# Kernel tuning notes

Measured on AMD Instinct MI355X. Metric: run time of the kernel, lower is better.

## Reference

```python
import jax, jax.numpy as jnp
import numpy as np
from math import factorial

LMAX = 2
M_TOT = (LMAX + 1) ** 2  # 9 real spherical-harmonic components
CUTOFF = 5.0
N_RBF = 20

# ---------- Clebsch-Gordan coefficients in the real-SH basis (static) ----------

def _cg(j1, m1, j2, m2, j3, m3):
    if m1 + m2 != m3 or not (abs(j1 - j2) <= j3 <= j1 + j2):
        return 0.0
    f = factorial
    pre = ((2 * j3 + 1) * f(j1 + j2 - j3) * f(j1 - j2 + j3) * f(-j1 + j2 + j3) / f(j1 + j2 + j3 + 1)) ** 0.5
    pre *= (f(j3 + m3) * f(j3 - m3) * f(j1 - m1) * f(j1 + m1) * f(j2 - m2) * f(j2 + m2)) ** 0.5
    s = 0.0
    for k in range(j1 + j2 + j3 + 1):
        den = [k, j1 + j2 - j3 - k, j1 - m1 - k, j2 + m2 - k, j3 - j2 + m1 + k, j3 - j1 - m2 + k]
        if min(den) < 0:
            continue
        t = 1.0
        for dd in den:
            t *= f(dd)
        s += (-1) ** k / t
    return pre * s

def _u_real(l):
    # complex -> real SH change of basis, rows: real m, cols: complex m (offset by l)
    U = np.zeros((2 * l + 1, 2 * l + 1), dtype=complex)
    U[l, l] = 1.0
    s2 = 1.0 / np.sqrt(2.0)
    for m in range(1, l + 1):
        U[l + m, l + m] = (-1) ** m * s2
        U[l + m, l - m] = s2
        U[l - m, l - m] = 1j * s2
        U[l - m, l + m] = -1j * (-1) ** m * s2
    return U

def _build_cg_real(lmax):
    n = (lmax + 1) ** 2
    cg = np.zeros((n, n, n))
    for l1 in range(lmax + 1):
        for l2 in range(lmax + 1):
            for l3 in range(lmax + 1):
                if not (abs(l1 - l2) <= l3 <= l1 + l2):
                    continue
                C = np.zeros((2 * l1 + 1, 2 * l2 + 1, 2 * l3 + 1), dtype=complex)
                for m1 in range(-l1, l1 + 1):
                    for m2 in range(-l2, l2 + 1):
                        m3 = m1 + m2
                        if abs(m3) <= l3:
                            C[m1 + l1, m2 + l2, m3 + l3] = _cg(l1, m1, l2, m2, l3, m3)
                Cr = np.einsum('ai,bj,ck,ijk->abc', _u_real(l1), _u_real(l2), _u_real(l3).conj(), C)
                # odd-parity (l1+l2+l3 odd) entries are purely imaginary -> Re() zeroes them
                cg[l1 * l1:(l1 + 1) ** 2, l2 * l2:(l2 + 1) ** 2, l3 * l3:(l3 + 1) ** 2] = Cr.real
    return cg

_CGD = _build_cg_real(LMAX)
_mask = np.abs(_CGD) > 1e-10
_i1, _i2, _io = np.nonzero(_mask)
IDX1, IDX2, IDXO = jnp.array(_i1), jnp.array(_i2), jnp.array(_io)
CG_VALS = jnp.array(_CGD[_mask].astype(np.float32))
_LS = np.concatenate([np.full(2 * l + 1, l) for l in range(LMAX + 1)])  # l of each flat (l,m) index
FILTER_IDX = jnp.array(_LS[_i2])  # radial filter channel = l of the spherical-harmonic input
LIDX = jnp.array(_LS)

# ---------- real spherical harmonics up to l=2 ----------

def rsh(d):  # d: [E,3] unit directions, output [E,9] ordered (l,m): (0,0),(1,-1..1),(2,-2..2)
    x, y, z = d[:, 0], d[:, 1], d[:, 2]
    c0 = 0.28209479177387814   # 0.5*sqrt(1/pi)
    c1 = 0.4886025119029199    # sqrt(3/(4*pi))
    c2 = 1.0925484305920792    # 0.5*sqrt(15/pi)
    c20 = 0.31539156525252005  # 0.25*sqrt(5/pi)
    c22 = 0.5462742152960396   # 0.25*sqrt(15/pi)
    return jnp.stack([
        jnp.full_like(x, c0),
        c1 * y, c1 * z, c1 * x,
        c2 * x * y, c2 * y * z, c20 * (3.0 * z * z - 1.0), c2 * x * z, c22 * (x * x - y * y),
    ], axis=-1)


def _forward(atomic_numbers, r_ij, idx_i, idx_j, emb, filt_w, filt_b,
             mix1_w, mix2_w, mix3_w, gate_w, gate_b):
    N = atomic_numbers.shape[0]
    F = emb.shape[-1]
    d = jnp.linalg.norm(r_ij, axis=1, keepdims=True)          # [E,1]
    dir_ij = r_ij / d
    Y = rsh(dir_ij)                                           # [E,9]
    offsets = jnp.linspace(0.0, CUTOFF, N_RBF)                # GaussianRBF
    coeff = -0.5 / (offsets[1] - offsets[0]) ** 2
    radial = jnp.exp(coeff * (d - offsets[None, 0:1] * 0 - offsets) ** 2)  # [E,n_rbf]
    cut = 0.5 * (jnp.cos(d * jnp.pi / CUTOFF) + 1.0) * (d < CUTOFF)        # CosineCutoff [E,1]
    x0 = emb[atomic_numbers]                                  # [N,F]
    x = jnp.concatenate([x0[:, None, :], jnp.zeros((N, M_TOT - 1, F), x0.dtype)], axis=1)  # scalar2rsh
    n_layers = filt_w.shape[0]
    for li in range(n_layers):
        # SO3Convolution: radial filter per output l, CG-coupled gather/scatter over edges
        W = (radial @ filt_w[li] + filt_b[li]).reshape(-1, LMAX + 1, F) * cut[:, :, None]  # [E,3,F]
        xj = x[idx_j]                                          # [E,9,F]
        v = xj[:, IDX1] * Y[:, IDX2, None] * CG_VALS[None, :, None] * W[:, FILTER_IDX]     # [E,P,F]
        v = jnp.zeros((v.shape[0], M_TOT, F), v.dtype).at[:, IDXO].add(v)                  # [E,9,F]
        dx = jax.ops.segment_sum(v, idx_i, num_segments=N)     # scatter to atoms [N,9,F]
        # mixing1 + SO3TensorProduct
        ddx = dx @ mix1_w[li]
        p = dx[:, IDX1] * ddx[:, IDX2] * CG_VALS[None, :, None]
        p = jnp.zeros((N, M_TOT, F), dx.dtype).at[:, IDXO].add(p)
        dx = dx + p
        # mixing2, parametric gated nonlinearity, mixing3
        dx = dx @ mix2_w[li]
        h = (dx[:, 0] @ gate_w[li] + gate_b[li]).reshape(N, LMAX + 1, F)
        dx = dx * jax.nn.sigmoid(h[:, LIDX])
        dx = dx @ mix3_w[li]
        x = x + dx
    return x  # multipole representation [N,9,F]; scalar rep is x[:,0]


def setup_inputs() -> dict:
    key = jax.random.key(0)
    ks = jax.random.split(key, 12)
    N, E, F, NR, L, MAXZ = 10000, 100000, 32, N_RBF, 2, 100
    atomic_numbers = jax.random.randint(ks[0], (N,), 0, MAXZ)
    r_ij = jax.random.normal(ks[1], (E, 3), dtype=jnp.float32)
    idx_i = jax.random.randint(ks[2], (E,), 0, N)
    idx_j = jax.random.randint(ks[3], (E,), 0, N)
    emb = jax.random.normal(ks[4], (MAXZ, F), dtype=jnp.float32)
    emb = emb.at[0].set(0.0)  # padding_idx=0
    filt_w = jax.random.normal(ks[5], (L, NR, (LMAX + 1) * F), dtype=jnp.float32) / np.sqrt(NR)
    filt_b = jnp.zeros((L, (LMAX + 1) * F), dtype=jnp.float32)
    mix1_w = jax.random.normal(ks[6], (L, F, F), dtype=jnp.float32) / np.sqrt(F)
    mix2_w = jax.random.normal(ks[7], (L, F, F), dtype=jnp.float32) / np.sqrt(F)
    mix3_w = jax.random.normal(ks[8], (L, F, F), dtype=jnp.float32) / np.sqrt(F)
    gate_w = jax.random.normal(ks[9], (L, F, (LMAX + 1) * F), dtype=jnp.float32) / np.sqrt(F)
    gate_b = jnp.zeros((L, (LMAX + 1) * F), dtype=jnp.float32)
    return {"atomic_numbers": atomic_numbers, "r_ij": r_ij, "idx_i": idx_i, "idx_j": idx_j,
            "emb": emb, "filt_w": filt_w, "filt_b": filt_b, "mix1_w": mix1_w,
            "mix2_w": mix2_w, "mix3_w": mix3_w, "gate_w": gate_w, "gate_b": gate_b}


def reference(atomic_numbers, r_ij, idx_i, idx_j, emb, filt_w, filt_b,
              mix1_w, mix2_w, mix3_w, gate_w, gate_b):
    return _forward(atomic_numbers, r_ij, idx_i, idx_j, emb, filt_w, filt_b,
                    mix1_w, mix2_w, mix3_w, gate_w, gate_b)
```

## Files before the change

### kernel.cpp

```cpp
#include <hip/hip_runtime.h>
#include <math.h>

#define F 32
#define NRBF 20
#define MAXNZ 192
#define MAXG 160
#define PI_F 3.14159265358979323846f

typedef float f4a __attribute__((ext_vector_type(4), aligned(4)));

constexpr double cfact(int n) { double r = 1.0; for (int i = 2; i <= n; i++) r *= (double)i; return r; }
constexpr double csqrt(double x) {
    if (x <= 0.0) return 0.0;
    double r = x < 1.0 ? 1.0 : x;
    for (int i = 0; i < 80; i++) r = 0.5 * (r + x / r);
    return r;
}
constexpr int cabs_i(int x) { return x < 0 ? -x : x; }

constexpr double cg_c(int j1, int m1, int j2, int m2, int j3, int m3) {
    if (m1 + m2 != m3) return 0.0;
    if (j3 < cabs_i(j1 - j2) || j3 > j1 + j2) return 0.0;
    double pre = csqrt((2.0 * j3 + 1) * cfact(j1 + j2 - j3) * cfact(j1 - j2 + j3) *
                       cfact(-j1 + j2 + j3) / cfact(j1 + j2 + j3 + 1));
    pre *= csqrt(cfact(j3 + m3) * cfact(j3 - m3) * cfact(j1 - m1) * cfact(j1 + m1) *
                 cfact(j2 - m2) * cfact(j2 + m2));
    double s = 0.0;
    for (int k = 0; k <= j1 + j2 + j3; k++) {
        int d0 = k, d1 = j1 + j2 - j3 - k, d2 = j1 - m1 - k, d3 = j2 + m2 - k;
        int d4 = j3 - j2 + m1 + k, d5 = j3 - j1 - m2 + k;
        if (d0 < 0 || d1 < 0 || d2 < 0 || d3 < 0 || d4 < 0 || d5 < 0) continue;
        double t = cfact(d0) * cfact(d1) * cfact(d2) * cfact(d3) * cfact(d4) * cfact(d5);
        s += ((k & 1) ? -1.0 : 1.0) / t;
    }
    return pre * s;
}

struct U5 { double re[5][5]; double im[5][5]; };
constexpr U5 u_real(int l) {
    U5 u{};
    u.re[l][l] = 1.0;
    double s2 = 1.0 / csqrt(2.0);
    for (int m = 1; m <= l; m++) {
        double sgn = (m & 1) ? -1.0 : 1.0;
        u.re[l + m][l + m] = sgn * s2;
        u.re[l + m][l - m] = s2;
        u.im[l - m][l - m] = s2;
        u.im[l - m][l + m] = -sgn * s2;
    }
    return u;
}

struct Dense { double c[9][9][9]; };
constexpr Dense build_dense() {
    Dense D{};
    for (int l1 = 0; l1 <= 2; l1++)
        for (int l2 = 0; l2 <= 2; l2++)
            for (int l3 = 0; l3 <= 2; l3++) {
                if (l3 < cabs_i(l1 - l2) || l3 > l1 + l2) continue;
                U5 U1 = u_real(l1), U2 = u_real(l2), U3 = u_real(l3);
                int n1 = 2 * l1 + 1, n2 = 2 * l2 + 1, n3 = 2 * l3 + 1;
                for (int i = 0; i < n1; i++)
                    for (int j = 0; j < n2; j++) {
                        int k = (i - l1) + (j - l2) + l3;
                        if (k < 0 || k >= n3) continue;
                        double C = cg_c(l1, i - l1, l2, j - l2, l3, k - l3);
                        if (C == 0.0) continue;
                        int as[2] = {i, n1 - 1 - i}, bs[2] = {j, n2 - 1 - j}, cs[2] = {k, n3 - 1 - k};
                        int na = (as[0] == as[1]) ? 1 : 2;
                        int nb = (bs[0] == bs[1]) ? 1 : 2;
                        int nc = (cs[0] == cs[1]) ? 1 : 2;
                        for (int ai = 0; ai < na; ai++)
                            for (int bi = 0; bi < nb; bi++)
                                for (int ci = 0; ci < nc; ci++) {
                                    int aa = as[ai], bb = bs[bi], cc = cs[ci];
                                    double xr = U1.re[aa][i], xi = U1.im[aa][i];
                                    double yr = U2.re[bb][j], yi = U2.im[bb][j];
                                    double tr = xr * yr - xi * yi;
                                    double ti = xr * yi + xi * yr;
                                    double zr = U3.re[cc][k], zi = -U3.im[cc][k];
                                    double add = (tr * zr - ti * zi) * C;
                                    if (add != 0.0)
                                        D.c[l1 * l1 + aa][l2 * l2 + bb][l3 * l3 + cc] += add;
                                }
                    }
            }
    return D;
}

struct CgG {
    int nnz, ng;
    int goff[10];
    int gb[MAXG];
    int aoff[MAXG + 1];
    int aidx[MAXNZ];
    float aval[MAXNZ];
};
constexpr CgG build_g() {
    CgG t{};
    Dense D = build_dense();
    int g = 0, c = 0;
    for (int o = 0; o < 9; o++) {
        t.goff[o] = g;
        for (int b = 0; b < 9; b++) {
            bool any = false;
            for (int a = 0; a < 9; a++) {
                double v = D.c[a][b][o];
                if (v > 1e-10 || v < -1e-10) {
                    if (!any) { t.gb[g] = b; t.aoff[g] = c; any = true; }
                    t.aidx[c] = a; t.aval[c] = (float)v; c++;
                }
            }
            if (any) g++;
        }
    }
    t.goff[9] = g; t.aoff[g] = c; t.ng = g; t.nnz = c;
    return t;
}
constexpr CgG CGG = build_g();
static_assert(CGG.nnz <= MAXNZ, "nnz overflow");
static_assert(CGG.ng <= MAXG, "group overflow");

struct CgF { int cnt; int b[16]; int o[16]; float v[16]; };
constexpr CgF build_f() {
    CgF t{};
    Dense D = build_dense();
    int c = 0;
    for (int o = 0; o < 9; o++)
        for (int b = 0; b < 9; b++) {
            double v = D.c[0][b][o];
            if (v > 1e-10 || v < -1e-10) { t.b[c] = b; t.o[c] = o; t.v[c] = (float)v; c++; }
        }
    t.cnt = c;
    return t;
}
constexpr CgF CGF = build_f();
static_assert(CGF.cnt <= 16, "first-layer table overflow");

__device__ inline float readlane_f(float v, int lane) {
    union { float f; int i; } u; u.f = v;
    int r = __builtin_amdgcn_readlane(u.i, lane);
    union { int i; float f; } w; w.i = r;
    return w.f;
}


__global__ void init_x_kernel(float* __restrict__ x, const int* __restrict__ Z,
                              const float* __restrict__ emb, int N) {
    int t = blockIdx.x * blockDim.x + threadIdx.x;
    if (t >= N * F) return;
    int n = t >> 5, f = t & 31;
    float* xp = x + (size_t)n * 288 + f * 9;
    xp[0] = emb[Z[n] * F + f];
    #pragma unroll
    for (int m = 1; m < 9; m++) xp[m] = 0.0f;
}

__global__ void hist_kernel(const int* __restrict__ idx_i, int* __restrict__ deg, int E) {
    int e = blockIdx.x * blockDim.x + threadIdx.x;
    if (e < E) atomicAdd(&deg[idx_i[e]], 1);
}

#define SCAN_T 1024
__global__ __launch_bounds__(SCAN_T) void scan_kernel(
    const int* __restrict__ deg, int* __restrict__ rowptr,
    int* __restrict__ cursor, int N) {
    __shared__ int part[SCAN_T];
    int t = threadIdx.x;
    int per = (N + SCAN_T - 1) / SCAN_T;
    int lo = t * per, hi = lo + per;
    if (hi > N) hi = N;
    int s = 0;
    for (int i = lo; i < hi; i++) s += deg[i];
    part[t] = s;
    __syncthreads();
    for (int off = 1; off < SCAN_T; off <<= 1) {
        int v = (t >= off) ? part[t - off] : 0;
        __syncthreads();
        part[t] += v;
        __syncthreads();
    }
    int run = (t == 0) ? 0 : part[t - 1];
    for (int i = lo; i < hi; i++) {
        rowptr[i] = run;
        cursor[i] = run;
        run += deg[i];
    }
    if (t == SCAN_T - 1) rowptr[N] = run;
}

__global__ void scatter_kernel(const int* __restrict__ idx_i, const int* __restrict__ idx_j,
                               const float* __restrict__ rij, int* __restrict__ cursor,
                               int* __restrict__ jperm, float4* __restrict__ geomp,
                               float* __restrict__ radp, int E) {
    int e = blockIdx.x * blockDim.x + threadIdx.x;
    if (e >= E) return;
    int p = atomicAdd(&cursor[idx_i[e]], 1);
    jperm[p] = idx_j[e];
    float rx = rij[3 * e + 0], ry = rij[3 * e + 1], rz = rij[3 * e + 2];
    float d = sqrtf(rx * rx + ry * ry + rz * rz);
    float inv = 1.0f / d;
    float cu = (d < 5.0f) ? 0.5f * (__cosf(d * PI_F / 5.0f) + 1.0f) : 0.0f;
    geomp[p] = make_float4(rx * inv, ry * inv, rz * inv, cu);
    const float step = 5.0f / 19.0f;
    const float coeff = -0.5f / (step * step);
    float* rp = radp + (size_t)p * NRBF;
    #pragma unroll
    for (int r = 0; r < NRBF; r++) {
        float tt = d - step * (float)r;
        rp[r] = __expf(coeff * tt * tt);
    }
}

template <bool FIRST>
__global__ __launch_bounds__(256, 2) void layer_kernel(
    const float* __restrict__ xin, float* __restrict__ xout,
    const float* __restrict__ radp, const float4* __restrict__ geomp,
    const int* __restrict__ jperm, const int* __restrict__ rowptr,
    const float* __restrict__ fw, const float* __restrict__ fbias,
    const float* __restrict__ m1w, const float* __restrict__ m2w,
    const float* __restrict__ m3w,
    const float* __restrict__ gw, const float* __restrict__ gbias,
    int N, int std_out) {

    __shared__ float fwl[NRBF * 128];
    int tid = threadIdx.x;
    for (int idx = tid; idx < NRBF * 96; idx += 256) {
        int r = idx / 96, q = idx % 96, c = q >> 5, fq = q & 31;
        fwl[r * 128 + fq * 4 + c] = fw[idx];
    }
    __syncthreads();

    int lane = tid & 63;
    int h = lane >> 5;
    int f = lane & 31;
    int n = blockIdx.x * 4 + (tid >> 6);
    if (n >= N) return;

    float fb0 = fbias[f], fb1 = fbias[F + f], fb2 = fbias[2 * F + f];

    const float c0 = 0.28209479177387814f, c1 = 0.4886025119029199f;
    const float c2 = 1.0925484305920792f, c20 = 0.31539156525252005f;
    const float c22 = 0.5462742152960396f;

    float msg[9];
    #pragma unroll
    for (int o = 0; o < 9; o++) msg[o] = 0.0f;

    const float* fl = &fwl[f * 4];
    int k0 = rowptr[n], k1 = rowptr[n + 1];
    for (int k = k0 + h; k < k1; k += 2) {
        const float4* rq = (const float4*)(radp + (size_t)k * NRBF);
        float4 q0 = rq[0], q1 = rq[1], q2 = rq[2], q3 = rq[3], q4 = rq[4];
        float4 g4 = geomp[k];
        int j = jperm[k];

        float W0 = fb0, W1 = fb1, W2 = fb2;
        float rv[NRBF] = {q0.x, q0.y, q0.z, q0.w, q1.x, q1.y, q1.z, q1.w,
                          q2.x, q2.y, q2.z, q2.w, q3.x, q3.y, q3.z, q3.w,
                          q4.x, q4.y, q4.z, q4.w};
        #pragma unroll
        for (int r = 0; r < NRBF; r++) {
            float4 w = *(const float4*)(fl + r * 128);
            W0 = fmaf(rv[r], w.x, W0);
            W1 = fmaf(rv[r], w.y, W1);
            W2 = fmaf(rv[r], w.z, W2);
        }
        float cu = g4.w;
        W0 *= cu; W1 *= cu; W2 *= cu;

        float ux = g4.x, uy = g4.y, uz = g4.z;
        float T[9];
        T[0] = c0 * W0;
        T[1] = c1 * uy * W1;
        T[2] = c1 * uz * W1;
        T[3] = c1 * ux * W1;
        T[4] = c2 * ux * uy * W2;
        T[5] = c2 * uy * uz * W2;
        T[6] = c20 * (3.0f * uz * uz - 1.0f) * W2;
        T[7] = c2 * ux * uz * W2;
        T[8] = c22 * (ux * ux - uy * uy) * W2;

        const float* xjp = xin + (size_t)j * 288 + f * 9;
        if (FIRST) {
            float xj0 = xjp[0];
            #pragma unroll
            for (int t = 0; t < CGF.cnt; t++)
                msg[CGF.o[t]] = fmaf(xj0, T[CGF.b[t]] * CGF.v[t], msg[CGF.o[t]]);
        } else {
            f4a xa = *(const f4a*)(xjp);
            f4a xb = *(const f4a*)(xjp + 4);
            float xj[9] = {xa.x, xa.y, xa.z, xa.w, xb.x, xb.y, xb.z, xb.w, xjp[8]};
            #pragma unroll
            for (int o = 0; o < 9; o++) {
                float accO = msg[o];
                #pragma unroll
                for (int gi = CGG.goff[o]; gi < CGG.goff[o + 1]; gi++) {
                    int t0 = CGG.aoff[gi];
                    float s = CGG.aval[t0] * xj[CGG.aidx[t0]];
                    #pragma unroll
                    for (int t = t0 + 1; t < CGG.aoff[gi + 1]; t++)
                        s = fmaf(CGG.aval[t], xj[CGG.aidx[t]], s);
                    accO = fmaf(s, T[CGG.gb[gi]], accO);
                }
                msg[o] = accO;
            }
        }
    }

    #pragma unroll
    for (int o = 0; o < 9; o++)
        msg[o] += __shfl_xor(msg[o], 32, 64);

    float wreg[F];

    #pragma unroll
    for (int g = 0; g < F; g++) wreg[g] = m1w[g * F + f];
    float ddx[9];
    #pragma unroll
    for (int m = 0; m < 9; m++) ddx[m] = 0.0f;
    #pragma unroll
    for (int g = 0; g < F; g++) {
        #pragma unroll
        for (int m = 0; m < 9; m++)
            ddx[m] = fmaf(readlane_f(msg[m], g), wreg[g], ddx[m]);
    }

    float tr[9];
    #pragma unroll
    for (int o = 0; o < 9; o++) {
        float accO = msg[o];
        #pragma unroll
        for (int gi = CGG.goff[o]; gi < CGG.goff[o + 1]; gi++) {
            int t0 = CGG.aoff[gi];
            float s = CGG.aval[t0] * msg[CGG.aidx[t0]];
            #pragma unroll
            for (int t = t0 + 1; t < CGG.aoff[gi + 1]; t++)
                s = fmaf(CGG.aval[t], msg[CGG.aidx[t]], s);
            accO = fmaf(s, ddx[CGG.gb[gi]], accO);
        }
        tr[o] = accO;
    }

    #pragma unroll
    for (int g = 0; g < F; g++) wreg[g] = m2w[g * F + f];
    float dx2[9];
    #pragma unroll
    for (int m = 0; m < 9; m++) dx2[m] = 0.0f;
    #pragma unroll
    for (int g = 0; g < F; g++) {
        #pragma unroll
        for (int m = 0; m < 9; m++)
            dx2[m] = fmaf(readlane_f(tr[m], g), wreg[g], dx2[m]);
    }

    float ga0 = gbias[f], ga1 = gbias[F + f], ga2 = gbias[2 * F + f];
    #pragma unroll
    for (int g = 0; g < F; g++) {
        float s = readlane_f(dx2[0], g);
        ga0 = fmaf(s, gw[g * 96 + f], ga0);
        ga1 = fmaf(s, gw[g * 96 + F + f], ga1);
        ga2 = fmaf(s, gw[g * 96 + 2 * F + f], ga2);
    }
    float s0 = 1.0f / (1.0f + __expf(-ga0));
    float s1 = 1.0f / (1.0f + __expf(-ga1));
    float s2 = 1.0f / (1.0f + __expf(-ga2));

    float gt[9];
    gt[0] = dx2[0] * s0;
    gt[1] = dx2[1] * s1; gt[2] = dx2[2] * s1; gt[3] = dx2[3] * s1;
    gt[4] = dx2[4] * s2; gt[5] = dx2[5] * s2; gt[6] = dx2[6] * s2;
    gt[7] = dx2[7] * s2; gt[8] = dx2[8] * s2;

    #pragma unroll
    for (int g = 0; g < F; g++) wreg[g] = m3w[g * F + f];
    float outv[9];
    #pragma unroll
    for (int m = 0; m < 9; m++) outv[m] = 0.0f;
    #pragma unroll
    for (int g = 0; g < F; g++) {
        #pragma unroll
        for (int m = 0; m < 9; m++)
            outv[m] = fmaf(readlane_f(gt[m], g), wreg[g], outv[m]);
    }

    if (h == 0) {
        const float* xip = xin + (size_t)n * 288 + f * 9;
        f4a xa = *(const f4a*)(xip);
        f4a xb = *(const f4a*)(xip + 4);
        float xold[9] = {xa.x, xa.y, xa.z, xa.w, xb.x, xb.y, xb.z, xb.w, xip[8]};
        if (std_out) {
            float* xop = xout + (size_t)n * 288;
            #pragma unroll
            for (int m = 0; m < 9; m++)
                xop[m * F + f] = xold[m] + outv[m];
        } else {
            float* xop = xout + (size_t)n * 288 + f * 9;
            f4a oa, ob;
            oa.x = xold[0] + outv[0]; oa.y = xold[1] + outv[1];
            oa.z = xold[2] + outv[2]; oa.w = xold[3] + outv[3];
            ob.x = xold[4] + outv[4]; ob.y = xold[5] + outv[5];
            ob.z = xold[6] + outv[6]; ob.w = xold[7] + outv[7];
            *(f4a*)(xop) = oa;
            *(f4a*)(xop + 4) = ob;
            xop[8] = xold[8] + outv[8];
        }
    }
}

extern "C" void kernel_launch(void* const* d_in, const int* in_sizes, int n_in,
                              void* d_out, int out_size, void* d_ws, size_t ws_size,
                              hipStream_t stream) {
    int N = in_sizes[0];
    int E = in_sizes[2];
    int L = in_sizes[5] / (NRBF * 3 * F);

    const int* Z = (const int*)d_in[0];
    const float* rij = (const float*)d_in[1];
    const int* idx_i = (const int*)d_in[2];
    const int* idx_j = (const int*)d_in[3];
    const float* emb = (const float*)d_in[4];
    const float* filt_w = (const float*)d_in[5];
    const float* filt_b = (const float*)d_in[6];
    const float* m1w = (const float*)d_in[7];
    const float* m2w = (const float*)d_in[8];
    const float* m3w = (const float*)d_in[9];
    const float* gw = (const float*)d_in[10];
    const float* gb = (const float*)d_in[11];

    float* ws = (float*)d_ws;
    float* radp = ws;
    float4* geomp = (float4*)(radp + (size_t)E * NRBF);
    float* xA = (float*)(geomp + E);
    float* xB = xA + (size_t)N * 288;
    int* jperm = (int*)(xB + (size_t)N * 288);
    int* deg = jperm + E;
    int* rowptr = deg + N;
    int* cursor = rowptr + N + 1;

    init_x_kernel<<<(N * F + 255) / 256, 256, 0, stream>>>(xA, Z, emb, N);

    hipMemsetAsync(deg, 0, (size_t)N * sizeof(int), stream);
    hist_kernel<<<(E + 255) / 256, 256, 0, stream>>>(idx_i, deg, E);
    scan_kernel<<<1, SCAN_T, 0, stream>>>(deg, rowptr, cursor, N);
    scatter_kernel<<<(E + 255) / 256, 256, 0, stream>>>(idx_i, idx_j, rij, cursor,
                                                        jperm, geomp, radp, E);

    float* cur = xA;
    for (int li = 0; li < L; li++) {
        int last = (li == L - 1);
        float* nxt = last ? (float*)d_out : ((cur == xA) ? xB : xA);
        if (li == 0)
            layer_kernel<true><<<(N + 3) / 4, 256, 0, stream>>>(
                cur, nxt, radp, geomp, jperm, rowptr,
                filt_w, filt_b, m1w, m2w, m3w, gw, gb, N, last);
        else
            layer_kernel<false><<<(N + 3) / 4, 256, 0, stream>>>(
                cur, nxt, radp, geomp, jperm, rowptr,
                filt_w + (size_t)li * NRBF * 96, filt_b + (size_t)li * 96,
                m1w + (size_t)li * F * F, m2w + (size_t)li * F * F,
                m3w + (size_t)li * F * F, gw + (size_t)li * F * 96,
                gb + (size_t)li * 96, N, last);
        cur = nxt;
    }
}
```

Before: 188.2 us.

## Split per-node feature mixing across half-waves via LDS instead of readlane broadcasts

The three 32x32 feature-mixing matvecs and the gate projection previously broadcast each input value with scalar readlanes while the second half-wave duplicated all the work. Now the 9 components are staged in a per-wave LDS buffer, each half-wave handles 16 of the 32 input features using float4 LDS reads, and the two halves are combined with a cross-half shuffle. The change also raises the launch-bounds occupancy hint from 2 to 4 blocks and unrolls the edge loop by 2. Correctness depends on intra-wave lockstep ordering, enforced only by a compiler memory barrier. It also relies on unaligned float4 global loads now that the align-4 vector type is gone, and register caps may cause spills.

```diff
diff --git a/kernel.cpp b/kernel.cpp
--- a/kernel.cpp
+++ b/kernel.cpp
@@ -6,8 +6,6 @@
 #define MAXNZ 192
 #define MAXG 160
 #define PI_F 3.14159265358979323846f
-
-typedef float f4a __attribute__((ext_vector_type(4), aligned(4)));
 
 constexpr double cfact(int n) { double r = 1.0; for (int i = 2; i <= n; i++) r *= (double)i; return r; }
 constexpr double csqrt(double x) {
@@ -137,12 +135,7 @@
 constexpr CgF CGF = build_f();
 static_assert(CGF.cnt <= 16, "first-layer table overflow");
 
-__device__ inline float readlane_f(float v, int lane) {
-    union { float f; int i; } u; u.f = v;
-    int r = __builtin_amdgcn_readlane(u.i, lane);
-    union { int i; float f; } w; w.i = r;
-    return w.f;
-}
+#define CBAR() asm volatile("" ::: "memory")
 
 
 __global__ void init_x_kernel(float* __restrict__ x, const int* __restrict__ Z,
@@ -213,7 +206,7 @@
 }
 
 template <bool FIRST>
-__global__ __launch_bounds__(256, 2) void layer_kernel(
+__global__ __launch_bounds__(256, 4) void layer_kernel(
     const float* __restrict__ xin, float* __restrict__ xout,
     const float* __restrict__ radp, const float4* __restrict__ geomp,
     const int* __restrict__ jperm, const int* __restrict__ rowptr,
@@ -224,6 +217,7 @@
     int N, int std_out) {
 
     __shared__ float fwl[NRBF * 128];
+    __shared__ float dxs[4][9][F];
     int tid = threadIdx.x;
     for (int idx = tid; idx < NRBF * 96; idx += 256) {
         int r = idx / 96, q = idx % 96, c = q >> 5, fq = q & 31;
@@ -234,7 +228,8 @@
     int lane = tid & 63;
     int h = lane >> 5;
     int f = lane & 31;
-    int n = blockIdx.x * 4 + (tid >> 6);
+    int w = tid >> 6;
+    int n = blockIdx.x * 4 + w;
     if (n >= N) return;
 
     float fb0 = fbias[f], fb1 = fbias[F + f], fb2 = fbias[2 * F + f];
@@ -249,6 +244,7 @@
 
     const float* fl = &fwl[f * 4];
     int k0 = rowptr[n], k1 = rowptr[n + 1];
+    #pragma unroll 2
     for (int k = k0 + h; k < k1; k += 2) {
         const float4* rq = (const float4*)(radp + (size_t)k * NRBF);
         float4 q0 = rq[0], q1 = rq[1], q2 = rq[2], q3 = rq[3], q4 = rq[4];
@@ -261,10 +257,10 @@
                           q4.x, q4.y, q4.z, q4.w};
         #pragma unroll
         for (int r = 0; r < NRBF; r++) {
-            float4 w = *(const float4*)(fl + r * 128);
-            W0 = fmaf(rv[r], w.x, W0);
-            W1 = fmaf(rv[r], w.y, W1);
-            W2 = fmaf(rv[r], w.z, W2);
+            float4 wv = *(const float4*)(fl + r * 128);
+            W0 = fmaf(rv[r], wv.x, W0);
+            W1 = fmaf(rv[r], wv.y, W1);
+            W2 = fmaf(rv[r], wv.z, W2);
         }
         float cu = g4.w;
         W0 *= cu; W1 *= cu; W2 *= cu;
@@ -288,8 +284,8 @@
             for (int t = 0; t < CGF.cnt; t++)
                 msg[CGF.o[t]] = fmaf(xj0, T[CGF.b[t]] * CGF.v[t], msg[CGF.o[t]]);
         } else {
-            f4a xa = *(const f4a*)(xjp);
-            f4a xb = *(const f4a*)(xjp + 4);
+            float4 xa = *(const float4*)(xjp);
+            float4 xb = *(const float4*)(xjp + 4);
             float xj[9] = {xa.x, xa.y, xa.z, xa.w, xb.x, xb.y, xb.z, xb.w, xjp[8]};
             #pragma unroll
             for (int o = 0; o < 9; o++) {
@@ -312,19 +308,33 @@
     for (int o = 0; o < 9; o++)
         msg[o] += __shfl_xor(msg[o], 32, 64);
 
-    float wreg[F];
-
-    #pragma unroll
-    for (int g = 0; g < F; g++) wreg[g] = m1w[g * F + f];
+    const int gb0 = h * 4;
+    float wreg[16];
+
+    if (h == 0) {
+        #pragma unroll
+        for (int m = 0; m < 9; m++) dxs[w][m][f] = msg[m];
+    }
+    CBAR();
+
+    #pragma unroll
+    for (int gi = 0; gi < 16; gi++) wreg[gi] = m1w[(h * 16 + gi) * F + f];
     float ddx[9];
     #pragma unroll
-    for (int m = 0; m < 9; m++) ddx[m] = 0.0f;
-    #pragma unroll
-    for (int g = 0; g < F; g++) {
-        #pragma unroll
-        for (int m = 0; m < 9; m++)
-            ddx[m] = fmaf(readlane_f(msg[m], g), wreg[g], ddx[m]);
-    }
+    for (int m = 0; m < 9; m++) {
+        float acc = 0.0f;
+        #pragma unroll
+        for (int qb = 0; qb < 4; qb++) {
+            float4 dv = *(const float4*)&dxs[w][m][(gb0 + qb) * 4];
+            acc = fmaf(dv.x, wreg[qb * 4 + 0], acc);
+            acc = fmaf(dv.y, wreg[qb * 4 + 1], acc);
+            acc = fmaf(dv.z, wreg[qb * 4 + 2], acc);
+            acc = fmaf(dv.w, wreg[qb * 4 + 3], acc);
+        }
+        ddx[m] = acc;
+    }
+    #pragma unroll
+    for (int m = 0; m < 9; m++) ddx[m] += __shfl_xor(ddx[m], 32, 64);
 
     float tr[9];
     #pragma unroll
@@ -342,26 +352,51 @@
         tr[o] = accO;
     }
 
-    #pragma unroll
-    for (int g = 0; g < F; g++) wreg[g] = m2w[g * F + f];
+    CBAR();
+    if (h == 0) {
+        #pragma unroll
+        for (int m = 0; m < 9; m++) dxs[w][m][f] = tr[m];
+    }
+    CBAR();
+    #pragma unroll
+    for (int gi = 0; gi < 16; gi++) wreg[gi] = m2w[(h * 16 + gi) * F + f];
     float dx2[9];
     #pragma unroll
-    for (int m = 0; m < 9; m++) dx2[m] = 0.0f;
-    #pragma unroll
-    for (int g = 0; g < F; g++) {
-        #pragma unroll
-        for (int m = 0; m < 9; m++)
-            dx2[m] = fmaf(readlane_f(tr[m], g), wreg[g], dx2[m]);
-    }
-
-    float ga0 = gbias[f], ga1 = gbias[F + f], ga2 = gbias[2 * F + f];
-    #pragma unroll
-    for (int g = 0; g < F; g++) {
-        float s = readlane_f(dx2[0], g);
-        ga0 = fmaf(s, gw[g * 96 + f], ga0);
-        ga1 = fmaf(s, gw[g * 96 + F + f], ga1);
-        ga2 = fmaf(s, gw[g * 96 + 2 * F + f], ga2);
-    }
+    for (int m = 0; m < 9; m++) {
+        float acc = 0.0f;
+        #pragma unroll
+        for (int qb = 0; qb < 4; qb++) {
+            float4 dv = *(const float4*)&dxs[w][m][(gb0 + qb) * 4];
+            acc = fmaf(dv.x, wreg[qb * 4 + 0], acc);
+            acc = fmaf(dv.y, wreg[qb * 4 + 1], acc);
+            acc = fmaf(dv.z, wreg[qb * 4 + 2], acc);
+            acc = fmaf(dv.w, wreg[qb * 4 + 3], acc);
+        }
+        dx2[m] = acc;
+    }
+    #pragma unroll
+    for (int m = 0; m < 9; m++) dx2[m] += __shfl_xor(dx2[m], 32, 64);
+
+    CBAR();
+    if (h == 0) dxs[w][0][f] = dx2[0];
+    CBAR();
+    float ga0 = 0.0f, ga1 = 0.0f, ga2 = 0.0f;
+    #pragma unroll
+    for (int qb = 0; qb < 4; qb++) {
+        float4 sv = *(const float4*)&dxs[w][0][(gb0 + qb) * 4];
+        float sj[4] = {sv.x, sv.y, sv.z, sv.w};
+        #pragma unroll
+        for (int jj = 0; jj < 4; jj++) {
+            int g = h * 16 + qb * 4 + jj;
+            ga0 = fmaf(sj[jj], gw[g * 96 + f], ga0);
+            ga1 = fmaf(sj[jj], gw[g * 96 + F + f], ga1);
+            ga2 = fmaf(sj[jj], gw[g * 96 + 2 * F + f], ga2);
+        }
+    }
+    ga0 += __shfl_xor(ga0, 32, 64);
+    ga1 += __shfl_xor(ga1, 32, 64);
+    ga2 += __shfl_xor(ga2, 32, 64);
+    ga0 += gbias[f]; ga1 += gbias[F + f]; ga2 += gbias[2 * F + f];
     float s0 = 1.0f / (1.0f + __expf(-ga0));
     float s1 = 1.0f / (1.0f + __expf(-ga1));
     float s2 = 1.0f / (1.0f + __expf(-ga2));
@@ -372,22 +407,35 @@
     gt[4] = dx2[4] * s2; gt[5] = dx2[5] * s2; gt[6] = dx2[6] * s2;
     gt[7] = dx2[7] * s2; gt[8] = dx2[8] * s2;
 
-    #pragma unroll
-    for (int g = 0; g < F; g++) wreg[g] = m3w[g * F + f];
+    CBAR();
+    if (h == 0) {
+        #pragma unroll
+        for (int m = 0; m < 9; m++) dxs[w][m][f] = gt[m];
+    }
+    CBAR();
+    #pragma unroll
+    for (int gi = 0; gi < 16; gi++) wreg[gi] = m3w[(h * 16 + gi) * F + f];
     float outv[9];
     #pragma unroll
-    for (int m = 0; m < 9; m++) outv[m] = 0.0f;
-    #pragma unroll
-    for (int g = 0; g < F; g++) {
-        #pragma unroll
-        for (int m = 0; m < 9; m++)
-            outv[m] = fmaf(readlane_f(gt[m], g), wreg[g], outv[m]);
-    }
+    for (int m = 0; m < 9; m++) {
+        float acc = 0.0f;
+        #pragma unroll
+        for (int qb = 0; qb < 4; qb++) {
+            float4 dv = *(const float4*)&dxs[w][m][(gb0 + qb) * 4];
+            acc = fmaf(dv.x, wreg[qb * 4 + 0], acc);
+            acc = fmaf(dv.y, wreg[qb * 4 + 1], acc);
+            acc = fmaf(dv.z, wreg[qb * 4 + 2], acc);
+            acc = fmaf(dv.w, wreg[qb * 4 + 3], acc);
+        }
+        outv[m] = acc;
+    }
+    #pragma unroll
+    for (int m = 0; m < 9; m++) outv[m] += __shfl_xor(outv[m], 32, 64);
 
     if (h == 0) {
         const float* xip = xin + (size_t)n * 288 + f * 9;
-        f4a xa = *(const f4a*)(xip);
-        f4a xb = *(const f4a*)(xip + 4);
+        float4 xa = *(const float4*)(xip);
+        float4 xb = *(const float4*)(xip + 4);
         float xold[9] = {xa.x, xa.y, xa.z, xa.w, xb.x, xb.y, xb.z, xb.w, xip[8]};
         if (std_out) {
             float* xop = xout + (size_t)n * 288;
@@ -396,13 +444,13 @@
                 xop[m * F + f] = xold[m] + outv[m];
         } else {
             float* xop = xout + (size_t)n * 288 + f * 9;
-            f4a oa, ob;
+            float4 oa, ob;
             oa.x = xold[0] + outv[0]; oa.y = xold[1] + outv[1];
             oa.z = xold[2] + outv[2]; oa.w = xold[3] + outv[3];
             ob.x = xold[4] + outv[4]; ob.y = xold[5] + outv[5];
             ob.z = xold[6] + outv[6]; ob.w = xold[7] + outv[7];
-            *(f4a*)(xop) = oa;
-            *(f4a*)(xop + 4) = ob;
+            *(float4*)(xop) = oa;
+            *(float4*)(xop + 4) = ob;
             xop[8] = xold[8] + outv[8];
         }
     }
```

After: 402.4 us. 2.14x slower.
